# Kernel tuning notes

Measured on AMD Instinct MI355X. Metric: run time of the kernel, lower is better.

The kernel has to match this reference:

```python
import jax, jax.numpy as jnp
import numpy as np

N, K = 50000, 64          # nodes, anchors per node
E = N * K                 # anchor-set edges
IN_DIM, OUT_DIM = 256, 64


def setup_inputs() -> dict:
    key = jax.random.key(0)
    ks = jax.random.split(key, 12)
    s = 0.02
    return {
        "feature": jax.random.normal(ks[0], (N, IN_DIM), jnp.float32),
        "src": jax.random.randint(ks[1], (E,), 0, N),
        "dst": jax.random.randint(ks[2], (E,), 0, N),
        "sp_dist": jax.random.uniform(ks[3], (E, 1), jnp.float32),
        "anchor_eid": jax.random.randint(ks[4], (N * K,), 0, E),
        "dists_max": jax.random.uniform(ks[5], (N, K), jnp.float32),
        "W_u": jax.random.normal(ks[6], (IN_DIM, OUT_DIM), jnp.float32) * s,
        "b_u": jnp.zeros((OUT_DIM,), jnp.float32),
        "W_v": jax.random.normal(ks[7], (IN_DIM, OUT_DIM), jnp.float32) * s,
        "b_v": jnp.zeros((OUT_DIM,), jnp.float32),
        "W_out": jax.random.normal(ks[8], (OUT_DIM, 1), jnp.float32) * s,
        "b_out": jnp.zeros((1,), jnp.float32),
    }


def reference(feature, src, dst, sp_dist, anchor_eid, dists_max,
              W_u, b_u, W_v, b_v, W_out, b_out):
    # node-level linear projections: [N, OUT_DIM]
    u_feat = feature @ W_u + b_u
    v_feat = feature @ W_v + b_v
    # edge message: v_feat[dst] + u_feat[src] * sp_dist  -> [E, OUT_DIM]
    message = v_feat[dst] + u_feat[src] * sp_dist
    # gather anchor edges and reshape to [N, K, OUT_DIM]
    msgs = jax.nn.relu(
        message[anchor_eid].reshape(dists_max.shape[0], dists_max.shape[1], -1)
    )
    out_position = (msgs @ W_out + b_out)[..., 0]  # [N, K]
    out_structure = jnp.mean(msgs, axis=1)         # [N, OUT_DIM]
    return out_position, out_structure
```

## Files before the change

kernel.cpp:

```cpp
#include <hip/hip_runtime.h>
#include <hip/hip_fp16.h>
#include <hip/hip_bf16.h>


#define IN_DIM 256
#define OUT_DIM 64
#define KANCH 64

typedef float vfloat4 __attribute__((ext_vector_type(4)));
typedef float vfloat2 __attribute__((ext_vector_type(2)));

__global__ __launch_bounds__(256) void pgnn_merge_init_kernel(
    const int* __restrict__ src, const int* __restrict__ dst,
    const float* __restrict__ sp, unsigned long long* __restrict__ meta, int E,
    float* __restrict__ out_pos, const float* __restrict__ b_out, int M,
    int mergeBlocks)
{
    if ((int)blockIdx.x < mergeBlocks) {
        int i = blockIdx.x * 256 + threadIdx.x;
        if (i >= E) return;
        unsigned long long pk =
              (unsigned long long)(unsigned)__builtin_nontemporal_load(&src[i])
            | ((unsigned long long)(unsigned)__builtin_nontemporal_load(&dst[i]) << 17)
            | ((unsigned long long)__half_as_ushort(
                   __float2half_rn(__builtin_nontemporal_load(&sp[i]))) << 34);
        __builtin_nontemporal_store(pk, &meta[i]);
    } else {
        const float bo = b_out[0];
        int i4 = (blockIdx.x - mergeBlocks) * 256 + threadIdx.x;
        int base = i4 * 4;
        if (base + 3 < M) {
            vfloat4 s = {bo, bo, bo, bo};
            __builtin_nontemporal_store(s, reinterpret_cast<vfloat4*>(&out_pos[base]));
        } else {
            for (int i = base; i < M; ++i) out_pos[i] = bo;
        }
    }
}

#define PAa 68
#define PBb 132
#define TILEF (16 * PAa + 16 * PBb)
__global__ __launch_bounds__(256) void pgnn_fused_kernel(
    const float* __restrict__ feature,
    const float* __restrict__ Wu, const float* __restrict__ bu,
    const float* __restrict__ Wv, const float* __restrict__ bv,
    unsigned char* __restrict__ uq8,
    __half* __restrict__ vh16,
    const int* __restrict__ aeid,
    const unsigned long long* __restrict__ meta,
    unsigned long long* __restrict__ packed,
    int N, int M, int projBlocks, int packBlocks)
{
    __shared__ float smem[2 * TILEF];
    const int tid = threadIdx.x;

    if ((int)blockIdx.x < projBlocks) {
        const int row0 = blockIdx.x * 64;
        const int tr = tid >> 4;
        const int tc = tid & 15;
        const int mA = tid >> 2, c4A = tid & 3;
        const int grA = row0 + mA;

        float accU[4][4], accV[4][4];
        #pragma unroll
        for (int i = 0; i < 4; ++i)
            #pragma unroll
            for (int j = 0; j < 4; ++j) { accU[i][j] = 0.f; accV[i][j] = 0.f; }

        float4 ra, rb0, rb1;
        auto load_tile = [&](int k0) {
            ra = make_float4(0.f, 0.f, 0.f, 0.f);
            if (grA < N)
                ra = *reinterpret_cast<const float4*>(
                        &feature[(size_t)grA * IN_DIM + k0 + c4A * 4]);
            {
                int f = tid, kk = f >> 5, c4 = f & 31;
                rb0 = (c4 < 16)
                    ? *reinterpret_cast<const float4*>(&Wu[(k0 + kk) * OUT_DIM + c4 * 4])
                    : *reinterpret_cast<const float4*>(&Wv[(k0 + kk) * OUT_DIM + (c4 - 16) * 4]);
            }
            {
                int f = tid + 256, kk = f >> 5, c4 = f & 31;
                rb1 = (c4 < 16)
                    ? *reinterpret_cast<const float4*>(&Wu[(k0 + kk) * OUT_DIM + c4 * 4])
                    : *reinterpret_cast<const float4*>(&Wv[(k0 + kk) * OUT_DIM + (c4 - 16) * 4]);
            }
        };
        auto store_tile = [&](float* buf) {
            buf[(c4A * 4 + 0) * PAa + mA] = ra.x;
            buf[(c4A * 4 + 1) * PAa + mA] = ra.y;
            buf[(c4A * 4 + 2) * PAa + mA] = ra.z;
            buf[(c4A * 4 + 3) * PAa + mA] = ra.w;
            float* sB = buf + 16 * PAa;
            {
                int f = tid, kk = f >> 5, c4 = f & 31;
                *reinterpret_cast<float4*>(&sB[kk * PBb + c4 * 4]) = rb0;
            }
            {
                int f = tid + 256, kk = f >> 5, c4 = f & 31;
                *reinterpret_cast<float4*>(&sB[kk * PBb + c4 * 4]) = rb1;
            }
        };

        load_tile(0);
        store_tile(smem);
        __syncthreads();

        for (int s = 0; s < 16; ++s) {
            const int cur = s & 1;
            if (s < 15) load_tile((s + 1) * 16);
            const float* buf = smem + cur * TILEF;
            const float* sB  = buf + 16 * PAa;
            #pragma unroll
            for (int k = 0; k < 16; ++k) {
                float4 a  = *reinterpret_cast<const float4*>(&buf[k * PAa + tr * 4]);
                float4 b0 = *reinterpret_cast<const float4*>(&sB[k * PBb + tc * 4]);
                float4 b1 = *reinterpret_cast<const float4*>(&sB[k * PBb + 64 + tc * 4]);
                float av[4]  = {a.x, a.y, a.z, a.w};
                float bu4[4] = {b0.x, b0.y, b0.z, b0.w};
                float bv4[4] = {b1.x, b1.y, b1.z, b1.w};
                #pragma unroll
                for (int i = 0; i < 4; ++i)
                    #pragma unroll
                    for (int j = 0; j < 4; ++j) {
                        accU[i][j] = fmaf(av[i], bu4[j], accU[i][j]);
                        accV[i][j] = fmaf(av[i], bv4[j], accV[i][j]);
                    }
            }
            if (s < 15) store_tile(smem + (cur ^ 1) * TILEF);
            __syncthreads();
        }

        const int qs   = tc >> 3;
        const int offq = (tc & 7) * 4;
        float bU[4], bV[4];
        #pragma unroll
        for (int j = 0; j < 4; ++j) { bU[j] = bu[tc * 4 + j]; bV[j] = bv[tc * 4 + j]; }
        #pragma unroll
        for (int i = 0; i < 4; ++i) {
            int gr = row0 + tr * 4 + i;
            if (gr >= N) continue;
            unsigned char* urow = uq8 + ((size_t)qs * N + gr) * 32;
            int pu = 0;
            pu = __builtin_amdgcn_cvt_pk_fp8_f32(accU[i][0] + bU[0],
                                                 accU[i][1] + bU[1], pu, false);
            pu = __builtin_amdgcn_cvt_pk_fp8_f32(accU[i][2] + bU[2],
                                                 accU[i][3] + bU[3], pu, true);
            *reinterpret_cast<unsigned int*>(urow + offq) = (unsigned)pu;

            __half* vrow = vh16 + ((size_t)qs * N + gr) * 32;
            __half2 hv0 = __floats2half2_rn(accV[i][0] + bV[0], accV[i][1] + bV[1]);
            __half2 hv1 = __floats2half2_rn(accV[i][2] + bV[2], accV[i][3] + bV[3]);
            *reinterpret_cast<__half2*>(vrow + offq)     = hv0;
            *reinterpret_cast<__half2*>(vrow + offq + 2) = hv1;
        }
    } else {
        const int stride = packBlocks * 256;
        int i = (blockIdx.x - projBlocks) * 256 + tid;
        while (i + 7 * stride < M) {
            int e[8];
            #pragma unroll
            for (int b = 0; b < 8; ++b)
                e[b] = __builtin_nontemporal_load(&aeid[i + b * stride]);
            unsigned long long m[8];
            #pragma unroll
            for (int b = 0; b < 8; ++b) m[b] = meta[e[b]];
            #pragma unroll
            for (int b = 0; b < 8; ++b)
                __builtin_nontemporal_store(m[b], &packed[i + b * stride]);
            i += 8 * stride;
        }
        for (; i < M; i += stride) {
            int e = __builtin_nontemporal_load(&aeid[i]);
            __builtin_nontemporal_store(meta[e], &packed[i]);
        }
    }
}

template<bool GATHER>
__global__ __launch_bounds__(256) void pgnn_pass2_kernel(
    const unsigned char* __restrict__ uq8,
    const __half* __restrict__ vh16,
    const int*    __restrict__ src,
    const int*    __restrict__ dst,
    const float*  __restrict__ sp_dist,
    const int*    __restrict__ aeid,
    const unsigned long long* __restrict__ packed,
    const float*  __restrict__ W_out,
    float* __restrict__ out_pos,
    float* __restrict__ out_struct,
    int N, int nblk)
{
    const int q   = blockIdx.x / nblk;
    const int blk = blockIdx.x - q * nblk;
    const int lane = threadIdx.x & 63;
    const int wv   = threadIdx.x >> 6;
    const int n    = blk * 4 + wv;
    if (n >= N) return;

    __shared__ float posb[4][64];
    float* pb = posb[wv];

    const int j = lane & 3, g = lane >> 2;

    int ms, md; float msp;
    if constexpr (GATHER) {
        const int e = __builtin_nontemporal_load(&aeid[(size_t)n * KANCH + lane]);
        ms = src[e]; md = dst[e]; msp = sp_dist[e];
    } else {
        unsigned long long pk =
            __builtin_nontemporal_load(&packed[(size_t)n * KANCH + lane]);
        unsigned lo = (unsigned)pk, hi = (unsigned)(pk >> 32);
        ms = (int)(lo & 0x1FFFFu);
        md = (int)(((lo >> 17) | (hi << 15)) & 0x1FFFFu);
        msp = __half2float(__ushort_as_half((unsigned short)((hi >> 2) & 0xFFFFu)));
    }

    float w[8];
    {
        const float* Wq = &W_out[q * 32 + j * 8];
        float4 w0 = *reinterpret_cast<const float4*>(Wq);
        float4 w1 = *reinterpret_cast<const float4*>(Wq + 4);
        w[0] = w0.x; w[1] = w0.y; w[2] = w0.z; w[3] = w0.w;
        w[4] = w1.x; w[5] = w1.y; w[6] = w1.z; w[7] = w1.w;
    }

    const unsigned char* Uq = uq8  + (size_t)q * N * 32;
    const __half*        Vq = vh16 + (size_t)q * N * 32;

    float sacc[8];
    #pragma unroll
    for (int jj = 0; jj < 8; ++jj) sacc[jj] = 0.f;

    #pragma unroll
    for (int i = 0; i < 4; ++i) {
        const int k = i * 16 + g;
        const int   ss = __shfl(ms, k);
        const int   dd = __shfl(md, k);
        const float sp = __shfl(msp, k);

        uint2 uu = *reinterpret_cast<const uint2*>(Uq + (size_t)ss * 32 + j * 8);
        uint4 vv = *reinterpret_cast<const uint4*>(
                       reinterpret_cast<const unsigned char*>(Vq) +
                       (size_t)dd * 64 + j * 16);

        float uf[8], vf[8];
        {
            vfloat2 a0 = __builtin_amdgcn_cvt_pk_f32_fp8((int)uu.x, false);
            vfloat2 a1 = __builtin_amdgcn_cvt_pk_f32_fp8((int)uu.x, true);
            vfloat2 a2 = __builtin_amdgcn_cvt_pk_f32_fp8((int)uu.y, false);
            vfloat2 a3 = __builtin_amdgcn_cvt_pk_f32_fp8((int)uu.y, true);
            uf[0] = a0.x; uf[1] = a0.y; uf[2] = a1.x; uf[3] = a1.y;
            uf[4] = a2.x; uf[5] = a2.y; uf[6] = a3.x; uf[7] = a3.y;
        }
        {
            const unsigned* vp = &vv.x;
            #pragma unroll
            for (int t = 0; t < 4; ++t) {
                __half2 h2 = *reinterpret_cast<const __half2*>(&vp[t]);
                float2 f2 = __half22float2(h2);
                vf[2 * t] = f2.x; vf[2 * t + 1] = f2.y;
            }
        }

        float m[8];
        #pragma unroll
        for (int jj = 0; jj < 8; ++jj) {
            m[jj] = fmaxf(fmaf(uf[jj], sp, vf[jj]), 0.f);
            sacc[jj] += m[jj];
        }

        float p = 0.f;
        #pragma unroll
        for (int jj = 0; jj < 8; ++jj) p = fmaf(m[jj], w[jj], p);
        p += __shfl_xor(p, 1);
        p += __shfl_xor(p, 2);
        if (j == 0) pb[k] = p;
    }
    asm volatile("s_waitcnt lgkmcnt(0)" ::: "memory");

    atomicAdd(&out_pos[(size_t)n * KANCH + lane], pb[lane]);

    #pragma unroll
    for (int off = 4; off <= 32; off <<= 1)
        #pragma unroll
        for (int jj = 0; jj < 8; ++jj)
            sacc[jj] += __shfl_xor(sacc[jj], off);

    if (lane < 4) {
        const float r = 1.f / (float)KANCH;
        float* op = &out_struct[(size_t)n * OUT_DIM + q * 32 + lane * 8];
        vfloat4 s0 = { sacc[0] * r, sacc[1] * r, sacc[2] * r, sacc[3] * r };
        vfloat4 s1 = { sacc[4] * r, sacc[5] * r, sacc[6] * r, sacc[7] * r };
        __builtin_nontemporal_store(s0, reinterpret_cast<vfloat4*>(op));
        __builtin_nontemporal_store(s1, reinterpret_cast<vfloat4*>(op + 4));
    }
}

extern "C" void kernel_launch(void* const* d_in, const int* in_sizes, int n_in,
                              void* d_out, int out_size, void* d_ws, size_t ws_size,
                              hipStream_t stream) {
    const float* feature    = (const float*)d_in[0];
    const int*   src        = (const int*)  d_in[1];
    const int*   dst        = (const int*)  d_in[2];
    const float* sp_dist    = (const float*)d_in[3];
    const int*   anchor_eid = (const int*)  d_in[4];
    const float* W_u   = (const float*)d_in[6];
    const float* b_u   = (const float*)d_in[7];
    const float* W_v   = (const float*)d_in[8];
    const float* b_v   = (const float*)d_in[9];
    const float* W_out = (const float*)d_in[10];
    const float* b_out = (const float*)d_in[11];

    const int N = in_sizes[0] / IN_DIM;
    const int E = in_sizes[1];
    const int M = N * KANCH;

    unsigned char* uq8 = (unsigned char*)d_ws;
    size_t uq8_bytes  = (size_t)N * 64;
    size_t vh_off     = (uq8_bytes + 255) & ~(size_t)255;
    __half* vh16      = (__half*)((char*)d_ws + vh_off);
    size_t vh_bytes   = (size_t)N * 64 * sizeof(__half);
    size_t packed_off = (vh_off + vh_bytes + 255) & ~(size_t)255;
    size_t meta_off   = (packed_off + (size_t)M * 8 + 255) & ~(size_t)255;
    unsigned long long* packed = (unsigned long long*)((char*)d_ws + packed_off);
    unsigned long long* meta   = (unsigned long long*)((char*)d_ws + meta_off);
    const bool fields_fit = (N < (1 << 17));
    const bool use_packed = fields_fit && (ws_size >= meta_off + (size_t)E * 8);

    float* out_pos    = (float*)d_out;
    float* out_struct = (float*)d_out + (size_t)N * KANCH;

    const int projBlocks = (N + 63) / 64;
    const int nblk = (N + 3) / 4;
    const int initBlocks = ((M + 3) / 4 + 255) / 256;

    if (use_packed) {
        const int mergeBlocks = (E + 255) / 256;
        pgnn_merge_init_kernel<<<dim3(mergeBlocks + initBlocks), 256, 0, stream>>>(
            src, dst, sp_dist, meta, E, out_pos, b_out, M, mergeBlocks);
        const int packBlocks = 512;
        pgnn_fused_kernel<<<dim3(projBlocks + packBlocks), 256, 0, stream>>>(
            feature, W_u, b_u, W_v, b_v, uq8, vh16, anchor_eid, meta, packed,
            N, M, projBlocks, packBlocks);
        pgnn_pass2_kernel<false><<<dim3(2 * nblk), 256, 0, stream>>>(
            uq8, vh16, src, dst, sp_dist, anchor_eid, packed, W_out,
            out_pos, out_struct, N, nblk);
    } else {
        pgnn_merge_init_kernel<<<dim3(initBlocks), 256, 0, stream>>>(
            src, dst, sp_dist, meta, 0, out_pos, b_out, M, 0);
        pgnn_fused_kernel<<<dim3(projBlocks), 256, 0, stream>>>(
            feature, W_u, b_u, W_v, b_v, uq8, vh16, anchor_eid, meta, packed,
            N, M, projBlocks, 0);
        pgnn_pass2_kernel<true><<<dim3(2 * nblk), 256, 0, stream>>>(
            uq8, vh16, src, dst, sp_dist, anchor_eid, packed, W_out,
            out_pos, out_struct, N, nblk);
    }
}
```

Before: 207.0 us.

## Interleave anchor-meta gather with projection GEMM inside each block

Removes the separate pack blocks and has every projection block also gather meta[anchor_eid] for a contiguous 4096-entry chunk. The gather is split into two halves, each issued before eight GEMM k-steps and stored after them, so the random-gather latency is hidden behind FMA work. The cost is more live registers (eight 64-bit values plus indices) on top of the 32 accumulators. It also ties pack coverage to the number of projection blocks, which happens to match M here.

```diff
diff --git a/kernel.cpp b/kernel.cpp
--- a/kernel.cpp
+++ b/kernel.cpp
@@ -50,131 +50,143 @@
     const int* __restrict__ aeid,
     const unsigned long long* __restrict__ meta,
     unsigned long long* __restrict__ packed,
-    int N, int M, int projBlocks, int packBlocks)
+    int N, int Mp )
 {
     __shared__ float smem[2 * TILEF];
     const int tid = threadIdx.x;
 
-    if ((int)blockIdx.x < projBlocks) {
-        const int row0 = blockIdx.x * 64;
-        const int tr = tid >> 4;
-        const int tc = tid & 15;
-        const int mA = tid >> 2, c4A = tid & 3;
-        const int grA = row0 + mA;
-
-        float accU[4][4], accV[4][4];
-        #pragma unroll
-        for (int i = 0; i < 4; ++i)
+    const int row0 = blockIdx.x * 64;
+    const int tr = tid >> 4;
+    const int tc = tid & 15;
+    const int mA = tid >> 2, c4A = tid & 3;
+    const int grA = row0 + mA;
+    const int pbase = blockIdx.x * 4096 + tid;
+
+    float accU[4][4], accV[4][4];
+    #pragma unroll
+    for (int i = 0; i < 4; ++i)
+        #pragma unroll
+        for (int j = 0; j < 4; ++j) { accU[i][j] = 0.f; accV[i][j] = 0.f; }
+
+    float4 ra, rb0, rb1;
+    auto load_tile = [&](int k0) {
+        ra = make_float4(0.f, 0.f, 0.f, 0.f);
+        if (grA < N)
+            ra = *reinterpret_cast<const float4*>(
+                    &feature[(size_t)grA * IN_DIM + k0 + c4A * 4]);
+        {
+            int f = tid, kk = f >> 5, c4 = f & 31;
+            rb0 = (c4 < 16)
+                ? *reinterpret_cast<const float4*>(&Wu[(k0 + kk) * OUT_DIM + c4 * 4])
+                : *reinterpret_cast<const float4*>(&Wv[(k0 + kk) * OUT_DIM + (c4 - 16) * 4]);
+        }
+        {
+            int f = tid + 256, kk = f >> 5, c4 = f & 31;
+            rb1 = (c4 < 16)
+                ? *reinterpret_cast<const float4*>(&Wu[(k0 + kk) * OUT_DIM + c4 * 4])
+                : *reinterpret_cast<const float4*>(&Wv[(k0 + kk) * OUT_DIM + (c4 - 16) * 4]);
+        }
+    };
+    auto store_tile = [&](float* buf) {
+        buf[(c4A * 4 + 0) * PAa + mA] = ra.x;
+        buf[(c4A * 4 + 1) * PAa + mA] = ra.y;
+        buf[(c4A * 4 + 2) * PAa + mA] = ra.z;
+        buf[(c4A * 4 + 3) * PAa + mA] = ra.w;
+        float* sB = buf + 16 * PAa;
+        {
+            int f = tid, kk = f >> 5, c4 = f & 31;
+            *reinterpret_cast<float4*>(&sB[kk * PBb + c4 * 4]) = rb0;
+        }
+        {
+            int f = tid + 256, kk = f >> 5, c4 = f & 31;
+            *reinterpret_cast<float4*>(&sB[kk * PBb + c4 * 4]) = rb1;
+        }
+    };
+    auto gemm_step = [&](int s) {
+        const int cur = s & 1;
+        if (s < 15) load_tile((s + 1) * 16);
+        const float* buf = smem + cur * TILEF;
+        const float* sB  = buf + 16 * PAa;
+        #pragma unroll
+        for (int k = 0; k < 16; ++k) {
+            float4 a  = *reinterpret_cast<const float4*>(&buf[k * PAa + tr * 4]);
+            float4 b0 = *reinterpret_cast<const float4*>(&sB[k * PBb + tc * 4]);
+            float4 b1 = *reinterpret_cast<const float4*>(&sB[k * PBb + 64 + tc * 4]);
+            float av[4]  = {a.x, a.y, a.z, a.w};
+            float bu4[4] = {b0.x, b0.y, b0.z, b0.w};
+            float bv4[4] = {b1.x, b1.y, b1.z, b1.w};
             #pragma unroll
-            for (int j = 0; j < 4; ++j) { accU[i][j] = 0.f; accV[i][j] = 0.f; }
-
-        float4 ra, rb0, rb1;
-        auto load_tile = [&](int k0) {
-            ra = make_float4(0.f, 0.f, 0.f, 0.f);
-            if (grA < N)
-                ra = *reinterpret_cast<const float4*>(
-                        &feature[(size_t)grA * IN_DIM + k0 + c4A * 4]);
-            {
-                int f = tid, kk = f >> 5, c4 = f & 31;
-                rb0 = (c4 < 16)
-                    ? *reinterpret_cast<const float4*>(&Wu[(k0 + kk) * OUT_DIM + c4 * 4])
-                    : *reinterpret_cast<const float4*>(&Wv[(k0 + kk) * OUT_DIM + (c4 - 16) * 4]);
-            }
-            {
-                int f = tid + 256, kk = f >> 5, c4 = f & 31;
-                rb1 = (c4 < 16)
-                    ? *reinterpret_cast<const float4*>(&Wu[(k0 + kk) * OUT_DIM + c4 * 4])
-                    : *reinterpret_cast<const float4*>(&Wv[(k0 + kk) * OUT_DIM + (c4 - 16) * 4]);
-            }
-        };
-        auto store_tile = [&](float* buf) {
-            buf[(c4A * 4 + 0) * PAa + mA] = ra.x;
-            buf[(c4A * 4 + 1) * PAa + mA] = ra.y;
-            buf[(c4A * 4 + 2) * PAa + mA] = ra.z;
-            buf[(c4A * 4 + 3) * PAa + mA] = ra.w;
-            float* sB = buf + 16 * PAa;
-            {
-                int f = tid, kk = f >> 5, c4 = f & 31;
-                *reinterpret_cast<float4*>(&sB[kk * PBb + c4 * 4]) = rb0;
-            }
-            {
-                int f = tid + 256, kk = f >> 5, c4 = f & 31;
-                *reinterpret_cast<float4*>(&sB[kk * PBb + c4 * 4]) = rb1;
-            }
-        };
-
-        load_tile(0);
-        store_tile(smem);
+            for (int i = 0; i < 4; ++i)
+                #pragma unroll
+                for (int j = 0; j < 4; ++j) {
+                    accU[i][j] = fmaf(av[i], bu4[j], accU[i][j]);
+                    accV[i][j] = fmaf(av[i], bv4[j], accV[i][j]);
+                }
+        }
+        if (s < 15) store_tile(smem + (cur ^ 1) * TILEF);
         __syncthreads();
-
-        for (int s = 0; s < 16; ++s) {
-            const int cur = s & 1;
-            if (s < 15) load_tile((s + 1) * 16);
-            const float* buf = smem + cur * TILEF;
-            const float* sB  = buf + 16 * PAa;
-            #pragma unroll
-            for (int k = 0; k < 16; ++k) {
-                float4 a  = *reinterpret_cast<const float4*>(&buf[k * PAa + tr * 4]);
-                float4 b0 = *reinterpret_cast<const float4*>(&sB[k * PBb + tc * 4]);
-                float4 b1 = *reinterpret_cast<const float4*>(&sB[k * PBb + 64 + tc * 4]);
-                float av[4]  = {a.x, a.y, a.z, a.w};
-                float bu4[4] = {b0.x, b0.y, b0.z, b0.w};
-                float bv4[4] = {b1.x, b1.y, b1.z, b1.w};
-                #pragma unroll
-                for (int i = 0; i < 4; ++i)
-                    #pragma unroll
-                    for (int j = 0; j < 4; ++j) {
-                        accU[i][j] = fmaf(av[i], bu4[j], accU[i][j]);
-                        accV[i][j] = fmaf(av[i], bv4[j], accV[i][j]);
-                    }
-            }
-            if (s < 15) store_tile(smem + (cur ^ 1) * TILEF);
-            __syncthreads();
-        }
-
-        const int qs   = tc >> 3;
-        const int offq = (tc & 7) * 4;
-        float bU[4], bV[4];
-        #pragma unroll
-        for (int j = 0; j < 4; ++j) { bU[j] = bu[tc * 4 + j]; bV[j] = bv[tc * 4 + j]; }
-        #pragma unroll
-        for (int i = 0; i < 4; ++i) {
-            int gr = row0 + tr * 4 + i;
-            if (gr >= N) continue;
-            unsigned char* urow = uq8 + ((size_t)qs * N + gr) * 32;
-            int pu = 0;
-            pu = __builtin_amdgcn_cvt_pk_fp8_f32(accU[i][0] + bU[0],
-                                                 accU[i][1] + bU[1], pu, false);
-            pu = __builtin_amdgcn_cvt_pk_fp8_f32(accU[i][2] + bU[2],
-                                                 accU[i][3] + bU[3], pu, true);
-            *reinterpret_cast<unsigned int*>(urow + offq) = (unsigned)pu;
-
-            __half* vrow = vh16 + ((size_t)qs * N + gr) * 32;
-            __half2 hv0 = __floats2half2_rn(accV[i][0] + bV[0], accV[i][1] + bV[1]);
-            __half2 hv1 = __floats2half2_rn(accV[i][2] + bV[2], accV[i][3] + bV[3]);
-            *reinterpret_cast<__half2*>(vrow + offq)     = hv0;
-            *reinterpret_cast<__half2*>(vrow + offq + 2) = hv1;
-        }
-    } else {
-        const int stride = packBlocks * 256;
-        int i = (blockIdx.x - projBlocks) * 256 + tid;
-        while (i + 7 * stride < M) {
-            int e[8];
-            #pragma unroll
-            for (int b = 0; b < 8; ++b)
-                e[b] = __builtin_nontemporal_load(&aeid[i + b * stride]);
-            unsigned long long m[8];
-            #pragma unroll
-            for (int b = 0; b < 8; ++b) m[b] = meta[e[b]];
-            #pragma unroll
-            for (int b = 0; b < 8; ++b)
-                __builtin_nontemporal_store(m[b], &packed[i + b * stride]);
-            i += 8 * stride;
-        }
-        for (; i < M; i += stride) {
-            int e = __builtin_nontemporal_load(&aeid[i]);
-            __builtin_nontemporal_store(meta[e], &packed[i]);
-        }
+    };
+
+    load_tile(0);
+    store_tile(smem);
+    __syncthreads();
+
+    int e8[8]; unsigned long long m8[8];
+    #pragma unroll
+    for (int r = 0; r < 8; ++r) {
+        int idx = pbase + r * 256;
+        e8[r] = (idx < Mp) ? __builtin_nontemporal_load(&aeid[idx]) : -1;
+    }
+    #pragma unroll
+    for (int r = 0; r < 8; ++r)
+        m8[r] = (e8[r] >= 0) ? meta[e8[r]] : 0ull;
+
+    for (int s = 0; s < 8; ++s) gemm_step(s);
+
+    #pragma unroll
+    for (int r = 0; r < 8; ++r) {
+        int idx = pbase + r * 256;
+        if (idx < Mp) __builtin_nontemporal_store(m8[r], &packed[idx]);
+    }
+    #pragma unroll
+    for (int r = 0; r < 8; ++r) {
+        int idx = pbase + (8 + r) * 256;
+        e8[r] = (idx < Mp) ? __builtin_nontemporal_load(&aeid[idx]) : -1;
+    }
+    #pragma unroll
+    for (int r = 0; r < 8; ++r)
+        m8[r] = (e8[r] >= 0) ? meta[e8[r]] : 0ull;
+
+    for (int s = 8; s < 16; ++s) gemm_step(s);
+
+    #pragma unroll
+    for (int r = 0; r < 8; ++r) {
+        int idx = pbase + (8 + r) * 256;
+        if (idx < Mp) __builtin_nontemporal_store(m8[r], &packed[idx]);
+    }
+
+    const int qs   = tc >> 3;
+    const int offq = (tc & 7) * 4;
+    float bU[4], bV[4];
+    #pragma unroll
+    for (int j = 0; j < 4; ++j) { bU[j] = bu[tc * 4 + j]; bV[j] = bv[tc * 4 + j]; }
+    #pragma unroll
+    for (int i = 0; i < 4; ++i) {
+        int gr = row0 + tr * 4 + i;
+        if (gr >= N) continue;
+        unsigned char* urow = uq8 + ((size_t)qs * N + gr) * 32;
+        int pu = 0;
+        pu = __builtin_amdgcn_cvt_pk_fp8_f32(accU[i][0] + bU[0],
+                                             accU[i][1] + bU[1], pu, false);
+        pu = __builtin_amdgcn_cvt_pk_fp8_f32(accU[i][2] + bU[2],
+                                             accU[i][3] + bU[3], pu, true);
+        *reinterpret_cast<unsigned int*>(urow + offq) = (unsigned)pu;
+
+        __half* vrow = vh16 + ((size_t)qs * N + gr) * 32;
+        __half2 hv0 = __floats2half2_rn(accV[i][0] + bV[0], accV[i][1] + bV[1]);
+        __half2 hv1 = __floats2half2_rn(accV[i][2] + bV[2], accV[i][3] + bV[3]);
+        *reinterpret_cast<__half2*>(vrow + offq)     = hv0;
+        *reinterpret_cast<__half2*>(vrow + offq + 2) = hv1;
     }
 }
 
@@ -340,10 +352,9 @@
         const int mergeBlocks = (E + 255) / 256;
         pgnn_merge_init_kernel<<<dim3(mergeBlocks + initBlocks), 256, 0, stream>>>(
             src, dst, sp_dist, meta, E, out_pos, b_out, M, mergeBlocks);
-        const int packBlocks = 512;
-        pgnn_fused_kernel<<<dim3(projBlocks + packBlocks), 256, 0, stream>>>(
+        pgnn_fused_kernel<<<dim3(projBlocks), 256, 0, stream>>>(
             feature, W_u, b_u, W_v, b_v, uq8, vh16, anchor_eid, meta, packed,
-            N, M, projBlocks, packBlocks);
+            N, M);
         pgnn_pass2_kernel<false><<<dim3(2 * nblk), 256, 0, stream>>>(
             uq8, vh16, src, dst, sp_dist, anchor_eid, packed, W_out,
             out_pos, out_struct, N, nblk);
@@ -352,7 +363,7 @@
             src, dst, sp_dist, meta, 0, out_pos, b_out, M, 0);
         pgnn_fused_kernel<<<dim3(projBlocks), 256, 0, stream>>>(
             feature, W_u, b_u, W_v, b_v, uq8, vh16, anchor_eid, meta, packed,
-            N, M, projBlocks, 0);
+            N, 0 );
         pgnn_pass2_kernel<true><<<dim3(2 * nblk), 256, 0, stream>>>(
             uq8, vh16, src, dst, sp_dist, anchor_eid, packed, W_out,
             out_pos, out_struct, N, nblk);
```

After: 237.4 us. +14.7%, slower.

## Fuse anchor-meta packing into first pass and drop out_pos init kernel

Applied to the files above, without the earlier changes.

The projection GEMM and the edge-meta merge now run together in one front kernel. The anchor-eid gather of packed meta moves into the first half-column pass, which also writes out_pos directly with the bias. The second pass reads the packed buffer and accumulates into out_pos atomically. This removes the separate init fill and the standalone pack stage, at the cost of splitting the former single pass2 launch into two sequential launches, one per half of the output columns.

```diff
diff --git a/kernel.cpp b/kernel.cpp
--- a/kernel.cpp
+++ b/kernel.cpp
@@ -10,14 +10,25 @@
 typedef float vfloat4 __attribute__((ext_vector_type(4)));
 typedef float vfloat2 __attribute__((ext_vector_type(2)));
 
-__global__ __launch_bounds__(256) void pgnn_merge_init_kernel(
+#define PAa 68
+#define PBb 132
+#define TILEF (16 * PAa + 16 * PBb)
+__global__ __launch_bounds__(256) void pgnn_front_kernel(
+    const float* __restrict__ feature,
+    const float* __restrict__ Wu, const float* __restrict__ bu,
+    const float* __restrict__ Wv, const float* __restrict__ bv,
+    unsigned char* __restrict__ uq8,
+    __half* __restrict__ vh16,
     const int* __restrict__ src, const int* __restrict__ dst,
-    const float* __restrict__ sp, unsigned long long* __restrict__ meta, int E,
-    float* __restrict__ out_pos, const float* __restrict__ b_out, int M,
-    int mergeBlocks)
+    const float* __restrict__ sp,
+    unsigned long long* __restrict__ meta,
+    int N, int E, int projBlocks)
 {
-    if ((int)blockIdx.x < mergeBlocks) {
-        int i = blockIdx.x * 256 + threadIdx.x;
+    __shared__ float smem[2 * TILEF];
+    const int tid = threadIdx.x;
+
+    if ((int)blockIdx.x >= projBlocks) {
+        int i = (blockIdx.x - projBlocks) * 256 + tid;
         if (i >= E) return;
         unsigned long long pk =
               (unsigned long long)(unsigned)__builtin_nontemporal_load(&src[i])
@@ -25,178 +36,129 @@
             | ((unsigned long long)__half_as_ushort(
                    __float2half_rn(__builtin_nontemporal_load(&sp[i]))) << 34);
         __builtin_nontemporal_store(pk, &meta[i]);
-    } else {
-        const float bo = b_out[0];
-        int i4 = (blockIdx.x - mergeBlocks) * 256 + threadIdx.x;
-        int base = i4 * 4;
-        if (base + 3 < M) {
-            vfloat4 s = {bo, bo, bo, bo};
-            __builtin_nontemporal_store(s, reinterpret_cast<vfloat4*>(&out_pos[base]));
-        } else {
-            for (int i = base; i < M; ++i) out_pos[i] = bo;
-        }
+        return;
+    }
+
+    const int row0 = blockIdx.x * 64;
+    const int tr = tid >> 4;
+    const int tc = tid & 15;
+    const int mA = tid >> 2, c4A = tid & 3;
+    const int grA = row0 + mA;
+
+    float accU[4][4], accV[4][4];
+    #pragma unroll
+    for (int i = 0; i < 4; ++i)
+        #pragma unroll
+        for (int j = 0; j < 4; ++j) { accU[i][j] = 0.f; accV[i][j] = 0.f; }
+
+    float4 ra, rb0, rb1;
+    auto load_tile = [&](int k0) {
+        ra = make_float4(0.f, 0.f, 0.f, 0.f);
+        if (grA < N)
+            ra = *reinterpret_cast<const float4*>(
+                    &feature[(size_t)grA * IN_DIM + k0 + c4A * 4]);
+        {
+            int f = tid, kk = f >> 5, c4 = f & 31;
+            rb0 = (c4 < 16)
+                ? *reinterpret_cast<const float4*>(&Wu[(k0 + kk) * OUT_DIM + c4 * 4])
+                : *reinterpret_cast<const float4*>(&Wv[(k0 + kk) * OUT_DIM + (c4 - 16) * 4]);
+        }
+        {
+            int f = tid + 256, kk = f >> 5, c4 = f & 31;
+            rb1 = (c4 < 16)
+                ? *reinterpret_cast<const float4*>(&Wu[(k0 + kk) * OUT_DIM + c4 * 4])
+                : *reinterpret_cast<const float4*>(&Wv[(k0 + kk) * OUT_DIM + (c4 - 16) * 4]);
+        }
+    };
+    auto store_tile = [&](float* buf) {
+        buf[(c4A * 4 + 0) * PAa + mA] = ra.x;
+        buf[(c4A * 4 + 1) * PAa + mA] = ra.y;
+        buf[(c4A * 4 + 2) * PAa + mA] = ra.z;
+        buf[(c4A * 4 + 3) * PAa + mA] = ra.w;
+        float* sB = buf + 16 * PAa;
+        {
+            int f = tid, kk = f >> 5, c4 = f & 31;
+            *reinterpret_cast<float4*>(&sB[kk * PBb + c4 * 4]) = rb0;
+        }
+        {
+            int f = tid + 256, kk = f >> 5, c4 = f & 31;
+            *reinterpret_cast<float4*>(&sB[kk * PBb + c4 * 4]) = rb1;
+        }
+    };
+
+    load_tile(0);
+    store_tile(smem);
+    __syncthreads();
+
+    for (int s = 0; s < 16; ++s) {
+        const int cur = s & 1;
+        if (s < 15) load_tile((s + 1) * 16);
+        const float* buf = smem + cur * TILEF;
+        const float* sB  = buf + 16 * PAa;
+        #pragma unroll
+        for (int k = 0; k < 16; ++k) {
+            float4 a  = *reinterpret_cast<const float4*>(&buf[k * PAa + tr * 4]);
+            float4 b0 = *reinterpret_cast<const float4*>(&sB[k * PBb + tc * 4]);
+            float4 b1 = *reinterpret_cast<const float4*>(&sB[k * PBb + 64 + tc * 4]);
+            float av[4]  = {a.x, a.y, a.z, a.w};
+            float bu4[4] = {b0.x, b0.y, b0.z, b0.w};
+            float bv4[4] = {b1.x, b1.y, b1.z, b1.w};
+            #pragma unroll
+            for (int i = 0; i < 4; ++i)
+                #pragma unroll
+                for (int j = 0; j < 4; ++j) {
+                    accU[i][j] = fmaf(av[i], bu4[j], accU[i][j]);
+                    accV[i][j] = fmaf(av[i], bv4[j], accV[i][j]);
+                }
+        }
+        if (s < 15) store_tile(smem + (cur ^ 1) * TILEF);
+        __syncthreads();
+    }
+
+    const int qs   = tc >> 3;
+    const int offq = (tc & 7) * 4;
+    float bU[4], bV[4];
+    #pragma unroll
+    for (int j = 0; j < 4; ++j) { bU[j] = bu[tc * 4 + j]; bV[j] = bv[tc * 4 + j]; }
+    #pragma unroll
+    for (int i = 0; i < 4; ++i) {
+        int gr = row0 + tr * 4 + i;
+        if (gr >= N) continue;
+        unsigned char* urow = uq8 + ((size_t)qs * N + gr) * 32;
+        int pu = 0;
+        pu = __builtin_amdgcn_cvt_pk_fp8_f32(accU[i][0] + bU[0],
+                                             accU[i][1] + bU[1], pu, false);
+        pu = __builtin_amdgcn_cvt_pk_fp8_f32(accU[i][2] + bU[2],
+                                             accU[i][3] + bU[3], pu, true);
+        *reinterpret_cast<unsigned int*>(urow + offq) = (unsigned)pu;
+
+        __half* vrow = vh16 + ((size_t)qs * N + gr) * 32;
+        __half2 hv0 = __floats2half2_rn(accV[i][0] + bV[0], accV[i][1] + bV[1]);
+        __half2 hv1 = __floats2half2_rn(accV[i][2] + bV[2], accV[i][3] + bV[3]);
+        *reinterpret_cast<__half2*>(vrow + offq)     = hv0;
+        *reinterpret_cast<__half2*>(vrow + offq + 2) = hv1;
     }
 }
 
-#define PAa 68
-#define PBb 132
-#define TILEF (16 * PAa + 16 * PBb)
-__global__ __launch_bounds__(256) void pgnn_fused_kernel(
-    const float* __restrict__ feature,
-    const float* __restrict__ Wu, const float* __restrict__ bu,
-    const float* __restrict__ Wv, const float* __restrict__ bv,
-    unsigned char* __restrict__ uq8,
-    __half* __restrict__ vh16,
-    const int* __restrict__ aeid,
-    const unsigned long long* __restrict__ meta,
-    unsigned long long* __restrict__ packed,
-    int N, int M, int projBlocks, int packBlocks)
-{
-    __shared__ float smem[2 * TILEF];
-    const int tid = threadIdx.x;
-
-    if ((int)blockIdx.x < projBlocks) {
-        const int row0 = blockIdx.x * 64;
-        const int tr = tid >> 4;
-        const int tc = tid & 15;
-        const int mA = tid >> 2, c4A = tid & 3;
-        const int grA = row0 + mA;
-
-        float accU[4][4], accV[4][4];
-        #pragma unroll
-        for (int i = 0; i < 4; ++i)
-            #pragma unroll
-            for (int j = 0; j < 4; ++j) { accU[i][j] = 0.f; accV[i][j] = 0.f; }
-
-        float4 ra, rb0, rb1;
-        auto load_tile = [&](int k0) {
-            ra = make_float4(0.f, 0.f, 0.f, 0.f);
-            if (grA < N)
-                ra = *reinterpret_cast<const float4*>(
-                        &feature[(size_t)grA * IN_DIM + k0 + c4A * 4]);
-            {
-                int f = tid, kk = f >> 5, c4 = f & 31;
-                rb0 = (c4 < 16)
-                    ? *reinterpret_cast<const float4*>(&Wu[(k0 + kk) * OUT_DIM + c4 * 4])
-                    : *reinterpret_cast<const float4*>(&Wv[(k0 + kk) * OUT_DIM + (c4 - 16) * 4]);
-            }
-            {
-                int f = tid + 256, kk = f >> 5, c4 = f & 31;
-                rb1 = (c4 < 16)
-                    ? *reinterpret_cast<const float4*>(&Wu[(k0 + kk) * OUT_DIM + c4 * 4])
-                    : *reinterpret_cast<const float4*>(&Wv[(k0 + kk) * OUT_DIM + (c4 - 16) * 4]);
-            }
-        };
-        auto store_tile = [&](float* buf) {
-            buf[(c4A * 4 + 0) * PAa + mA] = ra.x;
-            buf[(c4A * 4 + 1) * PAa + mA] = ra.y;
-            buf[(c4A * 4 + 2) * PAa + mA] = ra.z;
-            buf[(c4A * 4 + 3) * PAa + mA] = ra.w;
-            float* sB = buf + 16 * PAa;
-            {
-                int f = tid, kk = f >> 5, c4 = f & 31;
-                *reinterpret_cast<float4*>(&sB[kk * PBb + c4 * 4]) = rb0;
-            }
-            {
-                int f = tid + 256, kk = f >> 5, c4 = f & 31;
-                *reinterpret_cast<float4*>(&sB[kk * PBb + c4 * 4]) = rb1;
-            }
-        };
-
-        load_tile(0);
-        store_tile(smem);
-        __syncthreads();
-
-        for (int s = 0; s < 16; ++s) {
-            const int cur = s & 1;
-            if (s < 15) load_tile((s + 1) * 16);
-            const float* buf = smem + cur * TILEF;
-            const float* sB  = buf + 16 * PAa;
-            #pragma unroll
-            for (int k = 0; k < 16; ++k) {
-                float4 a  = *reinterpret_cast<const float4*>(&buf[k * PAa + tr * 4]);
-                float4 b0 = *reinterpret_cast<const float4*>(&sB[k * PBb + tc * 4]);
-                float4 b1 = *reinterpret_cast<const float4*>(&sB[k * PBb + 64 + tc * 4]);
-                float av[4]  = {a.x, a.y, a.z, a.w};
-                float bu4[4] = {b0.x, b0.y, b0.z, b0.w};
-                float bv4[4] = {b1.x, b1.y, b1.z, b1.w};
-                #pragma unroll
-                for (int i = 0; i < 4; ++i)
-                    #pragma unroll
-                    for (int j = 0; j < 4; ++j) {
-                        accU[i][j] = fmaf(av[i], bu4[j], accU[i][j]);
-                        accV[i][j] = fmaf(av[i], bv4[j], accV[i][j]);
-                    }
-            }
-            if (s < 15) store_tile(smem + (cur ^ 1) * TILEF);
-            __syncthreads();
-        }
-
-        const int qs   = tc >> 3;
-        const int offq = (tc & 7) * 4;
-        float bU[4], bV[4];
-        #pragma unroll
-        for (int j = 0; j < 4; ++j) { bU[j] = bu[tc * 4 + j]; bV[j] = bv[tc * 4 + j]; }
-        #pragma unroll
-        for (int i = 0; i < 4; ++i) {
-            int gr = row0 + tr * 4 + i;
-            if (gr >= N) continue;
-            unsigned char* urow = uq8 + ((size_t)qs * N + gr) * 32;
-            int pu = 0;
-            pu = __builtin_amdgcn_cvt_pk_fp8_f32(accU[i][0] + bU[0],
-                                                 accU[i][1] + bU[1], pu, false);
-            pu = __builtin_amdgcn_cvt_pk_fp8_f32(accU[i][2] + bU[2],
-                                                 accU[i][3] + bU[3], pu, true);
-            *reinterpret_cast<unsigned int*>(urow + offq) = (unsigned)pu;
-
-            __half* vrow = vh16 + ((size_t)qs * N + gr) * 32;
-            __half2 hv0 = __floats2half2_rn(accV[i][0] + bV[0], accV[i][1] + bV[1]);
-            __half2 hv1 = __floats2half2_rn(accV[i][2] + bV[2], accV[i][3] + bV[3]);
-            *reinterpret_cast<__half2*>(vrow + offq)     = hv0;
-            *reinterpret_cast<__half2*>(vrow + offq + 2) = hv1;
-        }
-    } else {
-        const int stride = packBlocks * 256;
-        int i = (blockIdx.x - projBlocks) * 256 + tid;
-        while (i + 7 * stride < M) {
-            int e[8];
-            #pragma unroll
-            for (int b = 0; b < 8; ++b)
-                e[b] = __builtin_nontemporal_load(&aeid[i + b * stride]);
-            unsigned long long m[8];
-            #pragma unroll
-            for (int b = 0; b < 8; ++b) m[b] = meta[e[b]];
-            #pragma unroll
-            for (int b = 0; b < 8; ++b)
-                __builtin_nontemporal_store(m[b], &packed[i + b * stride]);
-            i += 8 * stride;
-        }
-        for (; i < M; i += stride) {
-            int e = __builtin_nontemporal_load(&aeid[i]);
-            __builtin_nontemporal_store(meta[e], &packed[i]);
-        }
-    }
-}
-
-template<bool GATHER>
-__global__ __launch_bounds__(256) void pgnn_pass2_kernel(
+template<int META, bool FIRST>
+__global__ __launch_bounds__(256) void pgnn_pass_kernel(
     const unsigned char* __restrict__ uq8,
     const __half* __restrict__ vh16,
     const int*    __restrict__ src,
     const int*    __restrict__ dst,
     const float*  __restrict__ sp_dist,
     const int*    __restrict__ aeid,
-    const unsigned long long* __restrict__ packed,
+    unsigned long long* __restrict__ packed,
+    const unsigned long long* __restrict__ meta,
     const float*  __restrict__ W_out,
+    const float*  __restrict__ b_out,
     float* __restrict__ out_pos,
     float* __restrict__ out_struct,
-    int N, int nblk)
+    int N, int q)
 {
-    const int q   = blockIdx.x / nblk;
-    const int blk = blockIdx.x - q * nblk;
     const int lane = threadIdx.x & 63;
     const int wv   = threadIdx.x >> 6;
-    const int n    = blk * 4 + wv;
+    const int n    = blockIdx.x * 4 + wv;
     if (n >= N) return;
 
     __shared__ float posb[4][64];
@@ -205,12 +167,18 @@
     const int j = lane & 3, g = lane >> 2;
 
     int ms, md; float msp;
-    if constexpr (GATHER) {
+    if constexpr (META == 2) {
         const int e = __builtin_nontemporal_load(&aeid[(size_t)n * KANCH + lane]);
         ms = src[e]; md = dst[e]; msp = sp_dist[e];
     } else {
-        unsigned long long pk =
-            __builtin_nontemporal_load(&packed[(size_t)n * KANCH + lane]);
+        unsigned long long pk;
+        if constexpr (META == 1) {
+            const int e = __builtin_nontemporal_load(&aeid[(size_t)n * KANCH + lane]);
+            pk = meta[e];
+            __builtin_nontemporal_store(pk, &packed[(size_t)n * KANCH + lane]);
+        } else {
+            pk = __builtin_nontemporal_load(&packed[(size_t)n * KANCH + lane]);
+        }
         unsigned lo = (unsigned)pk, hi = (unsigned)(pk >> 32);
         ms = (int)(lo & 0x1FFFFu);
         md = (int)(((lo >> 17) | (hi << 15)) & 0x1FFFFu);
@@ -280,7 +248,11 @@
     }
     asm volatile("s_waitcnt lgkmcnt(0)" ::: "memory");
 
-    atomicAdd(&out_pos[(size_t)n * KANCH + lane], pb[lane]);
+    if constexpr (FIRST) {
+        out_pos[(size_t)n * KANCH + lane] = pb[lane] + b_out[0];
+    } else {
+        atomicAdd(&out_pos[(size_t)n * KANCH + lane], pb[lane]);
+    }
 
     #pragma unroll
     for (int off = 4; off <= 32; off <<= 1)
@@ -334,27 +306,27 @@
 
     const int projBlocks = (N + 63) / 64;
     const int nblk = (N + 3) / 4;
-    const int initBlocks = ((M + 3) / 4 + 255) / 256;
 
     if (use_packed) {
         const int mergeBlocks = (E + 255) / 256;
-        pgnn_merge_init_kernel<<<dim3(mergeBlocks + initBlocks), 256, 0, stream>>>(
-            src, dst, sp_dist, meta, E, out_pos, b_out, M, mergeBlocks);
-        const int packBlocks = 512;
-        pgnn_fused_kernel<<<dim3(projBlocks + packBlocks), 256, 0, stream>>>(
-            feature, W_u, b_u, W_v, b_v, uq8, vh16, anchor_eid, meta, packed,
-            N, M, projBlocks, packBlocks);
-        pgnn_pass2_kernel<false><<<dim3(2 * nblk), 256, 0, stream>>>(
-            uq8, vh16, src, dst, sp_dist, anchor_eid, packed, W_out,
-            out_pos, out_struct, N, nblk);
+        pgnn_front_kernel<<<dim3(projBlocks + mergeBlocks), 256, 0, stream>>>(
+            feature, W_u, b_u, W_v, b_v, uq8, vh16, src, dst, sp_dist, meta,
+            N, E, projBlocks);
+        pgnn_pass_kernel<1, true><<<dim3(nblk), 256, 0, stream>>>(
+            uq8, vh16, src, dst, sp_dist, anchor_eid, packed, meta, W_out,
+            b_out, out_pos, out_struct, N, 0);
+        pgnn_pass_kernel<0, false><<<dim3(nblk), 256, 0, stream>>>(
+            uq8, vh16, src, dst, sp_dist, anchor_eid, packed, meta, W_out,
+            b_out, out_pos, out_struct, N, 1);
     } else {
-        pgnn_merge_init_kernel<<<dim3(initBlocks), 256, 0, stream>>>(
-            src, dst, sp_dist, meta, 0, out_pos, b_out, M, 0);
-        pgnn_fused_kernel<<<dim3(projBlocks), 256, 0, stream>>>(
-            feature, W_u, b_u, W_v, b_v, uq8, vh16, anchor_eid, meta, packed,
-            N, M, projBlocks, 0);
-        pgnn_pass2_kernel<true><<<dim3(2 * nblk), 256, 0, stream>>>(
-            uq8, vh16, src, dst, sp_dist, anchor_eid, packed, W_out,
-            out_pos, out_struct, N, nblk);
+        pgnn_front_kernel<<<dim3(projBlocks), 256, 0, stream>>>(
+            feature, W_u, b_u, W_v, b_v, uq8, vh16, src, dst, sp_dist, meta,
+            N, 0 , projBlocks);
+        pgnn_pass_kernel<2, true><<<dim3(nblk), 256, 0, stream>>>(
+            uq8, vh16, src, dst, sp_dist, anchor_eid, packed, meta, W_out,
+            b_out, out_pos, out_struct, N, 0);
+        pgnn_pass_kernel<2, false><<<dim3(nblk), 256, 0, stream>>>(
+            uq8, vh16, src, dst, sp_dist, anchor_eid, packed, meta, W_out,
+            b_out, out_pos, out_struct, N, 1);
     }
 }
```

New measurement: 222.0 us. 7.2% more time.
